# Kernel tuning notes

Measured on AMD Instinct MI355X. Metric: run time of the kernel, lower is better.

Reference implementation:

```python
import jax, jax.numpy as jnp
import numpy as np

B, N, C, H = 8, 1024, 256, 8   # graphs, nodes per graph, channels, heads
E = 131072                      # edges (avg degree 16)
DK = C // H
EPS = 1e-5


def setup_inputs() -> dict:
    key = jax.random.key(0)
    ks = jax.random.split(key, 16)
    s = 1.0 / np.sqrt(C)
    d = {
        'x': jax.random.normal(ks[0], (B * N, C), jnp.float32),
        'edge_index': jax.random.randint(ks[1], (2, E), 0, B * N, dtype=jnp.int64),
        'sph': jax.random.uniform(ks[2], (B, 1, N, N), jnp.float32),
        # local conv (GraphConv-style): root + neighbor linear
        'Wr': jax.random.normal(ks[3], (C, C), jnp.float32) * s,
        'Wn': jax.random.normal(ks[4], (C, C), jnp.float32) * s,
        # attention in/out projections (4 Linears as in MultiheadAttention)
        'Wq': jax.random.normal(ks[5], (C, C), jnp.float32) * s,
        'bq': jnp.zeros((C,), jnp.float32),
        'Wk': jax.random.normal(ks[6], (C, C), jnp.float32) * s,
        'bk': jnp.zeros((C,), jnp.float32),
        'Wv': jax.random.normal(ks[7], (C, C), jnp.float32) * s,
        'bv': jnp.zeros((C,), jnp.float32),
        'Wo': jax.random.normal(ks[8], (C, C), jnp.float32) * s,
        'bo': jnp.zeros((C,), jnp.float32),
        # MLP: C -> 2C -> C
        'W1': jax.random.normal(ks[9], (C, 2 * C), jnp.float32) * s,
        'b1': jnp.zeros((2 * C,), jnp.float32),
        'W2': jax.random.normal(ks[10], (2 * C, C), jnp.float32) * (1.0 / np.sqrt(2 * C)),
        'b2': jnp.zeros((C,), jnp.float32),
        # three batch norms (affine)
        'gamma1': jnp.ones((C,), jnp.float32), 'beta1': jnp.zeros((C,), jnp.float32),
        'gamma2': jnp.ones((C,), jnp.float32), 'beta2': jnp.zeros((C,), jnp.float32),
        'gamma3': jnp.ones((C,), jnp.float32), 'beta3': jnp.zeros((C,), jnp.float32),
    }
    return d


def _bn(h, g, b):
    # BatchNorm1d (training mode): per-feature stats over all nodes
    m = h.mean(axis=0)
    v = h.var(axis=0)
    return (h - m) * jax.lax.rsqrt(v + EPS) * g + b


def reference(x, edge_index, sph, Wr, Wn, Wq, bq, Wk, bk, Wv, bv, Wo, bo,
              W1, b1, W2, b2, gamma1, beta1, gamma2, beta2, gamma3, beta3):
    src, dst = edge_index[0], edge_index[1]

    # 1) local MPNN branch: h = conv(x) + x, then norm1
    msg = (x @ Wn)[src]                                   # [E, C]
    agg = jax.ops.segment_sum(msg, dst, num_segments=B * N)
    h1 = _bn(x @ Wr + agg + x, gamma1, beta1)             # [BN, C]

    # 2) global sph-modulated attention branch (dense batch is a reshape:
    #    equal-size graphs -> mask all True)
    hd = x.reshape(B, N, C)
    q = (hd @ Wq + bq).reshape(B, N, H, DK).transpose(0, 2, 1, 3)  # [B,H,N,DK]
    k = (hd @ Wk + bk).reshape(B, N, H, DK).transpose(0, 2, 1, 3)
    v = (hd @ Wv + bv).reshape(B, N, H, DK).transpose(0, 2, 1, 3)
    scores = jnp.einsum('bhnd,bhmd->bhnm', q, k) * (1.0 / np.sqrt(DK))
    scores = scores * sph                                  # structural modulation
    p = jax.nn.softmax(scores, axis=-1)
    o = jnp.einsum('bhnm,bhmd->bhnd', p, v)                # [B,H,N,DK]
    o = o.transpose(0, 2, 1, 3).reshape(B * N, C) @ Wo + bo
    h2 = _bn(o + x, gamma2, beta2)

    # 3) sum branches, MLP residual, norm3
    out = h1 + h2
    out = out + (jax.nn.relu(out @ W1 + b1) @ W2 + b2)
    return _bn(out, gamma3, beta3)
```

## Files before the change

### kernel.cpp

```cpp
#include <hip/hip_runtime.h>
#include <hip/hip_bf16.h>

constexpr int Bg  = 8;
constexpr int Nn  = 1024;
constexpr int Cc  = 256;
constexpr int Hh  = 8;
constexpr int DKh = 32;
constexpr int Ee  = 131072;
constexpr int BNn = Bg * Nn;
#define EPSV 1e-5f

typedef __attribute__((ext_vector_type(8))) short bf16x8;
typedef __attribute__((ext_vector_type(4))) float f32x4;

static __device__ __forceinline__ unsigned short f2b(float v) {
    __hip_bfloat16 h = __float2bfloat16(v);
    return __builtin_bit_cast(unsigned short, h);
}
static __device__ __forceinline__ float b2f(unsigned short u) {
    unsigned int x = ((unsigned int)u) << 16;
    return __builtin_bit_cast(float, x);
}
static __device__ __forceinline__ bf16x8 ldb8(const unsigned short* p) {
    return *(const bf16x8*)p;
}

__global__ __launch_bounds__(256) void prep_k(
    const float* __restrict__ x, unsigned short* __restrict__ xcat,
    const float* __restrict__ Wr, const float* __restrict__ Wn,
    const float* __restrict__ Wq, const float* __restrict__ Wk,
    const float* __restrict__ Wv, const float* __restrict__ Wo,
    const float* __restrict__ W1, const float* __restrict__ W2,
    unsigned short* __restrict__ WcatT,
    unsigned short* __restrict__ WqT, unsigned short* __restrict__ WkT,
    unsigned short* __restrict__ WvT, unsigned short* __restrict__ WoT,
    unsigned short* __restrict__ W1T, unsigned short* __restrict__ W2T,
    const int* __restrict__ ei, int* __restrict__ deg)
{
    int blk = blockIdx.x;
    if (blk < 2048) {
        int i = (blk * 256 + threadIdx.x) * 4;
        float4 v = *(const float4*)(x + i);
        int r = i >> 8, c = i & 255;
        ushort4 pk;
        pk.x = f2b(v.x); pk.y = f2b(v.y); pk.z = f2b(v.z); pk.w = f2b(v.w);
        *(ushort4*)(xcat + (size_t)r * 512 + c) = pk;
    } else if (blk < 4608) {
        int idx = (blk - 2048) * 256 + threadIdx.x;
        if (idx < 131072) {
            int n = idx >> 9, k = idx & 511;
            float v = (k < 256) ? Wr[k * 256 + n] : Wn[(k - 256) * 256 + n];
            WcatT[((size_t)(n >> 4) * 16 + (k >> 5)) * 512 + (n & 15) * 32 + (k & 31)] = f2b(v);
        } else if (idx < 393216) {
            int l = idx - 131072;
            int wsel = l >> 16; l &= 65535;
            int n = l >> 8, kk = l & 255;
            const float* S = wsel == 0 ? Wq : wsel == 1 ? Wk : wsel == 2 ? Wv : Wo;
            unsigned short* D = wsel == 0 ? WqT : wsel == 1 ? WkT : wsel == 2 ? WvT : WoT;
            D[((size_t)(n >> 4) * 8 + (kk >> 5)) * 512 + (n & 15) * 32 + (kk & 31)]
                = f2b(S[kk * 256 + n]);
        } else if (idx < 524288) {
            int l = idx - 393216;
            int n = l >> 8, kk = l & 255;
            W1T[((size_t)(n >> 4) * 8 + (kk >> 5)) * 512 + (n & 15) * 32 + (kk & 31)]
                = f2b(W1[kk * 512 + n]);
        } else {
            int l = idx - 524288;
            int n = l >> 9, kk = l & 511;
            W2T[((size_t)(n >> 4) * 16 + (kk >> 5)) * 512 + (n & 15) * 32 + (kk & 31)]
                = f2b(W2[kk * 256 + n]);
        }
    } else {
        int e = (blk - 4608) * 256 + threadIdx.x;
        atomicAdd(&deg[ei[Ee + e]], 1);
    }
}

__global__ __launch_bounds__(256) void scan_k(
    const int* __restrict__ deg, int* __restrict__ rowst, int* __restrict__ cursor)
{
    __shared__ int partial[256];
    int t = threadIdx.x;
    int local[32];
    int s = 0;
    #pragma unroll
    for (int i = 0; i < 32; ++i) { local[i] = deg[i * 256 + t]; s += local[i]; }
    partial[t] = s;
    __syncthreads();
    for (int off = 1; off < 256; off <<= 1) {
        int v = (t >= off) ? partial[t - off] : 0;
        __syncthreads();
        partial[t] += v;
        __syncthreads();
    }
    int base = partial[t] - s;
    #pragma unroll
    for (int i = 0; i < 32; ++i) {
        int n = i * 256 + t;
        rowst[n] = base;
        cursor[n] = base;
        base += local[i];
    }
}

__global__ __launch_bounds__(256) void place_k(
    const int* __restrict__ ei, int* __restrict__ cursor, int* __restrict__ eidx)
{
    int e = blockIdx.x * 256 + threadIdx.x;
    int s = ei[e], d = ei[Ee + e];
    int pos = atomicAdd(&cursor[d], 1);
    eidx[pos] = s;
}

__global__ __launch_bounds__(256, 4) void gather_qkv_k(
    const float* __restrict__ x, const int* __restrict__ rowst,
    const int* __restrict__ deg, const int* __restrict__ eidx,
    unsigned short* __restrict__ xcat,
    const unsigned short* __restrict__ WT,
    const float* __restrict__ bq, const float* __restrict__ bk,
    const float* __restrict__ bv,
    unsigned short* __restrict__ qb, unsigned short* __restrict__ kb,
    unsigned short* __restrict__ vTb, float qscale)
{
    __shared__ unsigned short vtile[64][40];
    int blk = blockIdx.x;

    if (blk < 2048) {
        int n = blk * 4 + (threadIdx.x >> 6);
        int c4 = (threadIdx.x & 63) * 4;
        int b0 = rowst[n], d = deg[n];
        float4 acc = {0.f, 0.f, 0.f, 0.f};
        int i = 0;
        for (; i + 4 <= d; i += 4) {
            int s0 = eidx[b0 + i], s1 = eidx[b0 + i + 1];
            int s2 = eidx[b0 + i + 2], s3 = eidx[b0 + i + 3];
            ushort4 a0 = *(const ushort4*)(xcat + (size_t)s0 * 512 + c4);
            ushort4 a1 = *(const ushort4*)(xcat + (size_t)s1 * 512 + c4);
            ushort4 a2 = *(const ushort4*)(xcat + (size_t)s2 * 512 + c4);
            ushort4 a3 = *(const ushort4*)(xcat + (size_t)s3 * 512 + c4);
            acc.x += (b2f(a0.x) + b2f(a1.x)) + (b2f(a2.x) + b2f(a3.x));
            acc.y += (b2f(a0.y) + b2f(a1.y)) + (b2f(a2.y) + b2f(a3.y));
            acc.z += (b2f(a0.z) + b2f(a1.z)) + (b2f(a2.z) + b2f(a3.z));
            acc.w += (b2f(a0.w) + b2f(a1.w)) + (b2f(a2.w) + b2f(a3.w));
        }
        for (; i < d; ++i) {
            int s = eidx[b0 + i];
            ushort4 a = *(const ushort4*)(xcat + (size_t)s * 512 + c4);
            acc.x += b2f(a.x); acc.y += b2f(a.y);
            acc.z += b2f(a.z); acc.w += b2f(a.w);
        }
        ushort4 pk;
        pk.x = f2b(acc.x); pk.y = f2b(acc.y); pk.z = f2b(acc.z); pk.w = f2b(acc.w);
        *(ushort4*)(xcat + (size_t)n * 512 + 256 + c4) = pk;
        return;
    }

    int qblk = blk - 2048;
    const int n0 = (qblk % 12) * 64;
    const int m0 = (qblk / 12) * 32;
    const int t = threadIdx.x;
    const int wave = t >> 6, lane = t & 63;
    const int tl = lane & 15, g = lane >> 4;
    const int wr = wave >> 1, wc = wave & 1;
    const int which = n0 >> 8;
    const int lda = 512;

    f32x4 acc[2] = {};

    const unsigned short* a0 = xcat + (size_t)(m0 + wr * 16 + tl) * lda + g * 8;
    const unsigned short* b0 = WT + ((size_t)(n0 >> 4) + wc * 2) * 8 * 512 + tl * 32 + g * 8;
    const unsigned short* b1 = b0 + 8 * 512;

    for (int k0 = 0; k0 < 256; k0 += 32) {
        bf16x8 af  = ldb8(a0 + k0);
        bf16x8 bf0 = ldb8(b0 + (k0 >> 5) * 512), bf1 = ldb8(b1 + (k0 >> 5) * 512);
        acc[0] = __builtin_amdgcn_mfma_f32_16x16x32_bf16(af, bf0, acc[0], 0, 0, 0);
        acc[1] = __builtin_amdgcn_mfma_f32_16x16x32_bf16(af, bf1, acc[1], 0, 0, 0);
    }

    const float* bias = which == 0 ? bq : which == 1 ? bk : bv;
    const float sc = which == 0 ? qscale : 1.f;

    if (which == 0) {
        #pragma unroll
        for (int c16 = 0; c16 < 2; ++c16)
            #pragma unroll
            for (int reg = 0; reg < 4; ++reg) {
                int row = m0 + wr * 16 + g * 4 + reg;
                int col = (n0 & 255) + wc * 32 + c16 * 16 + tl;
                qb[(size_t)row * Cc + col] = f2b((acc[c16][reg] + bias[col]) * sc);
            }
    } else if (which == 1) {
        #pragma unroll
        for (int c16 = 0; c16 < 2; ++c16)
            #pragma unroll
            for (int reg = 0; reg < 4; ++reg) {
                int row = m0 + wr * 16 + g * 4 + reg;
                int col = (n0 & 255) + wc * 32 + c16 * 16 + tl;
                kb[((size_t)(row >> 4) * 8 + (col >> 5)) * 512
                   + (row & 15) * 32 + (col & 31)] = f2b(acc[c16][reg] + bias[col]);
            }
    } else {
        #pragma unroll
        for (int c16 = 0; c16 < 2; ++c16)
            #pragma unroll
            for (int reg = 0; reg < 4; ++reg) {
                int colL = wc * 32 + c16 * 16 + tl;
                int rowL = wr * 16 + g * 4 + reg;
                vtile[colL][rowL] = f2b(acc[c16][reg] + bias[(n0 & 255) + colL]);
            }
        __syncthreads();
        int clocal = t >> 2, q4 = t & 3;
        int colg = (n0 & 255) + clocal;
        int hh = colg >> 5, dd = colg & 31;
        int bg = m0 >> 10;
        int m_loc = (m0 & 1023) + q4 * 8;
        int mt64 = m_loc >> 6, ks = (m_loc >> 5) & 1, gg = (m_loc >> 3) & 3;
        int cg = dd >> 4, tlv = dd & 15;
        ushort4 u0 = *(ushort4*)&vtile[clocal][q4 * 8];
        ushort4 u1 = *(ushort4*)&vtile[clocal][q4 * 8 + 4];
        unsigned short* dst = vTb
            + (((size_t)(bg * Hh + hh) * 16 + mt64) * 2048)
            + ((size_t)((ks * 2 + cg) * 16 + tlv) * 32) + gg * 8;
        *(ushort4*)dst = u0;
        *(ushort4*)(dst + 4) = u1;
    }
}

__global__ __launch_bounds__(512, 8) void attn_h1_k(
    const unsigned short* __restrict__ q, const unsigned short* __restrict__ k,
    const unsigned short* __restrict__ vT, const float* __restrict__ sph,
    unsigned short* __restrict__ op0,
    const unsigned short* __restrict__ xcat, const unsigned short* __restrict__ WcatT,
    const float* __restrict__ x, unsigned short* __restrict__ h1preb,
    float* __restrict__ gsum, float* __restrict__ gsq)
{
    __shared__ float Sph[2][16][132];
    __shared__ unsigned short Ps[Hh][16][72];
    float* csum = (float*)&Ps[0][0][0];
    float* csq  = csum + 256;

    const int blk = blockIdx.x;
    const int t = threadIdx.x;
    const int wave = t >> 6;
    const int lane = t & 63;
    const int tl = lane & 15, g = lane >> 4;

    if (blk < 512) {
        const int b  = blk & 7;
        const int n0 = (blk >> 3) * 16;
        const int w  = wave;

        bf16x8 qf = ldb8(q + ((size_t)(b * Nn + n0 + tl)) * Cc + w * DKh + g * 8);

        float lsum = 0.f;
        f32x4 oacc[2] = {};

        const unsigned short* kfb = k + ((size_t)(b * 512 + w)) * 512 + tl * 32 + g * 8;
        const unsigned short* vfb = vT + ((size_t)(b * Hh + w) * 16) * 2048
                                     + (size_t)tl * 32 + g * 8;
        const float* sbase = sph + ((size_t)b * Nn + n0) * Nn;

        if (t < 256) {
            int r1 = t >> 4, c1 = (t & 15) * 8;
            const float* src = sbase + (size_t)r1 * Nn + c1;
            *(float4*)&Sph[0][r1][c1]     = *(const float4*)src;
            *(float4*)&Sph[0][r1][c1 + 4] = *(const float4*)(src + 4);
        }
        __syncthreads();

        int cur = 0;
        for (int it = 0; it < 8; ++it) {
            const int m0 = it * 128;
            if (it < 7 && t < 256) {
                int r1 = t >> 4, c1 = (t & 15) * 8;
                const float* src = sbase + (size_t)r1 * Nn + m0 + 128 + c1;
                *(float4*)&Sph[cur ^ 1][r1][c1]     = *(const float4*)src;
                *(float4*)&Sph[cur ^ 1][r1][c1 + 4] = *(const float4*)(src + 4);
            }

            #pragma unroll
            for (int half = 0; half < 2; ++half) {
                const int mh = m0 + half * 64;

                f32x4 st[4];
                #pragma unroll
                for (int mg = 0; mg < 4; ++mg) {
                    bf16x8 ka = ldb8(kfb + (size_t)((mh >> 4) + mg) * 4096);
                    f32x4 z = {0.f, 0.f, 0.f, 0.f};
                    st[mg] = __builtin_amdgcn_mfma_f32_16x16x32_bf16(ka, qf, z, 0, 0, 0);
                }

                #pragma unroll
                for (int mg = 0; mg < 4; ++mg) {
                    float4 sp = *(const float4*)&Sph[cur][tl][half * 64 + mg * 16 + g * 4];
                    float p0 = __builtin_amdgcn_exp2f(st[mg][0] * sp.x);
                    float p1 = __builtin_amdgcn_exp2f(st[mg][1] * sp.y);
                    float p2 = __builtin_amdgcn_exp2f(st[mg][2] * sp.z);
                    float p3 = __builtin_amdgcn_exp2f(st[mg][3] * sp.w);
                    lsum += (p0 + p1) + (p2 + p3);
                    ushort4 pk;
                    pk.x = f2b(p0); pk.y = f2b(p1); pk.z = f2b(p2); pk.w = f2b(p3);
                    *(ushort4*)&Ps[w][tl][mg * 16 + g * 4] = pk;
                }

                const unsigned short* vtile64 = vfb + (size_t)(mh >> 6) * 2048;
                #pragma unroll
                for (int ks = 0; ks < 2; ++ks) {
                    bf16x8 pa = ldb8(&Ps[w][tl][ks * 32 + g * 8]);
                    #pragma unroll
                    for (int cg = 0; cg < 2; ++cg) {
                        bf16x8 vb = ldb8(vtile64 + (size_t)(ks * 2 + cg) * 512);
                        oacc[cg] = __builtin_amdgcn_mfma_f32_16x16x32_bf16(pa, vb, oacc[cg], 0, 0, 0);
                    }
                }
            }

            __syncthreads();
            cur ^= 1;
        }

        lsum += __shfl_xor(lsum, 16);
        lsum += __shfl_xor(lsum, 32);
        float* shl = (float*)&Ps[w][0][0];
        if (g == 0) shl[tl] = lsum;
        #pragma unroll
        for (int r = 0; r < 4; ++r) {
            float inv = 1.f / shl[g * 4 + r];
            #pragma unroll
            for (int cg = 0; cg < 2; ++cg)
                op0[((size_t)(b * Nn + n0 + g * 4 + r)) * Cc + w * DKh + cg * 16 + tl]
                    = f2b(oacc[cg][r] * inv);
        }
        return;
    }

    const int wrg = wave >> 2;
    const int wcg = wave & 3;
    const int m0g = (blk - 512) * 32;
    const int N = Cc;

    if (t < 256) { csum[t] = 0.f; csq[t] = 0.f; }
    __syncthreads();

    f32x4 acc[4] = {};

    const unsigned short* a0 = xcat + (size_t)(m0g + wrg * 16 + tl) * 512 + g * 8;
    const unsigned short* bb = WcatT + (size_t)(wcg * 4) * 16 * 512 + tl * 32 + g * 8;

    for (int k0 = 0; k0 < 512; k0 += 32) {
        bf16x8 af = ldb8(a0 + k0);
        #pragma unroll
        for (int c16 = 0; c16 < 4; ++c16) {
            bf16x8 bf = ldb8(bb + ((size_t)c16 * 16 + (k0 >> 5)) * 512);
            acc[c16] = __builtin_amdgcn_mfma_f32_16x16x32_bf16(af, bf, acc[c16], 0, 0, 0);
        }
    }

    #pragma unroll
    for (int c16 = 0; c16 < 4; ++c16) {
        int col = wcg * 64 + c16 * 16 + tl;
        float ls = 0.f, lq = 0.f;
        #pragma unroll
        for (int reg = 0; reg < 4; ++reg) {
            int row = m0g + wrg * 16 + g * 4 + reg;
            size_t idx = (size_t)row * N + col;
            float v = acc[c16][reg] + x[idx];
            ls += v; lq += v * v;
            h1preb[idx] = f2b(v);
        }
        atomicAdd(&csum[col], ls);
        atomicAdd(&csq[col],  lq);
    }
    __syncthreads();
    if (t < 256) {
        atomicAdd(&gsum[t], csum[t]);
        atomicAdd(&gsq[t],  csq[t]);
    }
}

template<int TAG>
__global__ __launch_bounds__(256, 4) void gemm_mfma_k(
    const unsigned short* __restrict__ A, const unsigned short* __restrict__ WT,
    const float* __restrict__ bias, const unsigned short* __restrict__ addb,
    float* __restrict__ outf, unsigned short* __restrict__ outb,
    float* __restrict__ gsum, float* __restrict__ gsq,
    int M, int K, int lda, int N, int relu, float oscale)
{
    const int t = threadIdx.x;
    const int wave = t >> 6, lane = t & 63;
    const int tl = lane & 15, g = lane >> 4;
    const int wr = wave >> 1, wc = wave & 1;
    const int m0 = blockIdx.y * 32, n0 = blockIdx.x * 64;

    __shared__ float csum[64], csq[64];
    if (gsum) {
        if (t < 64) { csum[t] = 0.f; csq[t] = 0.f; }
        __syncthreads();
    }

    f32x4 acc[2] = {};

    const int kt = K >> 5;
    const unsigned short* a0 = A  + (size_t)(m0 + wr * 16 + tl) * lda + g * 8;
    const unsigned short* b0 = WT + ((size_t)(n0 >> 4) + wc * 2) * kt * 512 + tl * 32 + g * 8;
    const unsigned short* b1 = b0 + (size_t)kt * 512;

    for (int k0 = 0; k0 < K; k0 += 32) {
        bf16x8 af  = ldb8(a0 + k0);
        bf16x8 bf0 = ldb8(b0 + (k0 >> 5) * 512), bf1 = ldb8(b1 + (k0 >> 5) * 512);
        acc[0] = __builtin_amdgcn_mfma_f32_16x16x32_bf16(af, bf0, acc[0], 0, 0, 0);
        acc[1] = __builtin_amdgcn_mfma_f32_16x16x32_bf16(af, bf1, acc[1], 0, 0, 0);
    }

    #pragma unroll
    for (int c16 = 0; c16 < 2; ++c16) {
        int colL = wc * 32 + c16 * 16 + tl;
        int col  = n0 + colL;
        float ls = 0.f, lq = 0.f;
        #pragma unroll
        for (int reg = 0; reg < 4; ++reg) {
            int row = m0 + wr * 16 + g * 4 + reg;
            float v = acc[c16][reg];
            if (bias) v += bias[col];
            v *= oscale;
            size_t idx = (size_t)row * N + col;
            if (addb) v += b2f(addb[idx]);
            ls += v; lq += v * v;
            if (relu) v = fmaxf(v, 0.f);
            if (outf) outf[idx] = v;
            if (outb) outb[idx] = f2b(v);
        }
        if (gsum) { atomicAdd(&csum[colL], ls); atomicAdd(&csq[colL], lq); }
    }
    if (gsum) {
        __syncthreads();
        if (t < 64) {
            atomicAdd(&gsum[n0 + t], csum[t]);
            atomicAdd(&gsq[n0 + t],  csq[t]);
        }
    }
}

__global__ __launch_bounds__(256, 4) void gemm_attnA_k(
    const unsigned short* __restrict__ op0,
    const unsigned short* __restrict__ WT, const float* __restrict__ bias,
    const float* __restrict__ add1, unsigned short* __restrict__ h2preb,
    float* __restrict__ gsum, float* __restrict__ gsq)
{
    const int K = Cc, N = Cc;
    const int t = threadIdx.x;
    const int wave = t >> 6, lane = t & 63;
    const int tl = lane & 15, g = lane >> 4;
    const int wr = wave >> 1, wc = wave & 1;
    const int m0 = blockIdx.y * 32, n0 = blockIdx.x * 64;

    __shared__ float csum[64], csq[64];
    if (t < 64) { csum[t] = 0.f; csq[t] = 0.f; }
    __syncthreads();

    f32x4 acc[2] = {};

    const int arow = m0 + wr * 16 + tl;
    const unsigned short* a0b = op0 + (size_t)arow * K + g * 8;
    const unsigned short* b0 = WT + ((size_t)(n0 >> 4) + wc * 2) * 8 * 512 + tl * 32 + g * 8;
    const unsigned short* b1 = b0 + 8 * 512;

    for (int k0 = 0; k0 < K; k0 += 32) {
        bf16x8 af  = ldb8(a0b + k0);
        bf16x8 bf0 = ldb8(b0 + (k0 >> 5) * 512), bf1 = ldb8(b1 + (k0 >> 5) * 512);
        acc[0] = __builtin_amdgcn_mfma_f32_16x16x32_bf16(af, bf0, acc[0], 0, 0, 0);
        acc[1] = __builtin_amdgcn_mfma_f32_16x16x32_bf16(af, bf1, acc[1], 0, 0, 0);
    }

    #pragma unroll
    for (int c16 = 0; c16 < 2; ++c16) {
        int colL = wc * 32 + c16 * 16 + tl;
        int col  = n0 + colL;
        float ls = 0.f, lq = 0.f;
        #pragma unroll
        for (int reg = 0; reg < 4; ++reg) {
            int row = m0 + wr * 16 + g * 4 + reg;
            float v = acc[c16][reg] + bias[col];
            size_t idx = (size_t)row * N + col;
            v += add1[idx];
            ls += v; lq += v * v;
            h2preb[idx] = f2b(v);
        }
        atomicAdd(&csum[colL], ls); atomicAdd(&csq[colL], lq);
    }
    __syncthreads();
    if (t < 64) {
        atomicAdd(&gsum[n0 + t], csum[t]);
        atomicAdd(&gsq[n0 + t],  csq[t]);
    }
}

__global__ __launch_bounds__(256) void bn_apply_k(
    const float* __restrict__ h, const float* __restrict__ gsum,
    const float* __restrict__ gsq, const float* __restrict__ gamma,
    const float* __restrict__ beta, float* __restrict__ outf)
{
    size_t i4 = ((size_t)blockIdx.x * 256 + threadIdx.x) * 4;
    int ch = (int)(i4 & (Cc - 1));
    float4 hv = *(const float4*)(h + i4);
    float4 sm = *(const float4*)(gsum + ch);
    float4 sq = *(const float4*)(gsq + ch);
    float4 ga = *(const float4*)(gamma + ch);
    float4 be = *(const float4*)(beta + ch);
    float4 o;
    {
        float m = sm.x * (1.f / BNn), var = sq.x * (1.f / BNn) - m * m;
        o.x = (hv.x - m) * rsqrtf(var + EPSV) * ga.x + be.x;
    }
    {
        float m = sm.y * (1.f / BNn), var = sq.y * (1.f / BNn) - m * m;
        o.y = (hv.y - m) * rsqrtf(var + EPSV) * ga.y + be.y;
    }
    {
        float m = sm.z * (1.f / BNn), var = sq.z * (1.f / BNn) - m * m;
        o.z = (hv.z - m) * rsqrtf(var + EPSV) * ga.z + be.z;
    }
    {
        float m = sm.w * (1.f / BNn), var = sq.w * (1.f / BNn) - m * m;
        o.w = (hv.w - m) * rsqrtf(var + EPSV) * ga.w + be.w;
    }
    *(float4*)(outf + i4) = o;
}

__global__ __launch_bounds__(256) void bn_apply12_k(
    const unsigned short* __restrict__ h1preb, const unsigned short* __restrict__ h2preb,
    const float* __restrict__ stats,
    const float* __restrict__ g1, const float* __restrict__ be1,
    const float* __restrict__ g2, const float* __restrict__ be2,
    unsigned short* __restrict__ outb)
{
    size_t i4 = ((size_t)blockIdx.x * 256 + threadIdx.x) * 4;
    int ch = (int)(i4 & (Cc - 1));
    ushort4 u1 = *(const ushort4*)(h1preb + i4);
    ushort4 u2 = *(const ushort4*)(h2preb + i4);
    float4 s1m = *(const float4*)(stats + ch);
    float4 s1q = *(const float4*)(stats + 256 + ch);
    float4 s2m = *(const float4*)(stats + 512 + ch);
    float4 s2q = *(const float4*)(stats + 768 + ch);
    float4 G1 = *(const float4*)(g1 + ch),  B1 = *(const float4*)(be1 + ch);
    float4 G2 = *(const float4*)(g2 + ch),  B2 = *(const float4*)(be2 + ch);
    ushort4 pk;
    #define BN12C(comp, ucomp) { \
        float m1 = s1m.comp * (1.f / BNn), v1 = s1q.comp * (1.f / BNn) - m1 * m1; \
        float m2 = s2m.comp * (1.f / BNn), v2 = s2q.comp * (1.f / BNn) - m2 * m2; \
        float o = (b2f(u1.ucomp) - m1) * rsqrtf(v1 + EPSV) * G1.comp + B1.comp \
                + (b2f(u2.ucomp) - m2) * rsqrtf(v2 + EPSV) * G2.comp + B2.comp; \
        pk.ucomp = f2b(o); }
    BN12C(x, x) BN12C(y, y) BN12C(z, z) BN12C(w, w)
    #undef BN12C
    *(ushort4*)(outb + i4) = pk;
}

extern "C" void kernel_launch(void* const* d_in, const int* in_sizes, int n_in,
                              void* d_out, int out_size, void* d_ws, size_t ws_size,
                              hipStream_t stream)
{
    const float* x   = (const float*)d_in[0];
    const int*   ei  = (const int*)  d_in[1];
    const float* sph = (const float*)d_in[2];
    const float* Wr  = (const float*)d_in[3];
    const float* Wn  = (const float*)d_in[4];
    const float* Wq  = (const float*)d_in[5];
    const float* bq  = (const float*)d_in[6];
    const float* Wk  = (const float*)d_in[7];
    const float* bk  = (const float*)d_in[8];
    const float* Wv  = (const float*)d_in[9];
    const float* bv  = (const float*)d_in[10];
    const float* Wo  = (const float*)d_in[11];
    const float* bo  = (const float*)d_in[12];
    const float* W1  = (const float*)d_in[13];
    const float* b1  = (const float*)d_in[14];
    const float* W2  = (const float*)d_in[15];
    const float* b2  = (const float*)d_in[16];
    const float* g1  = (const float*)d_in[17];
    const float* be1 = (const float*)d_in[18];
    const float* g2  = (const float*)d_in[19];
    const float* be2 = (const float*)d_in[20];
    const float* g3  = (const float*)d_in[21];
    const float* be3 = (const float*)d_in[22];
    float* out = (float*)d_out;

    const size_t SL = (size_t)BNn * Cc;

    float* ws = (float*)d_ws;
    float* s1 = ws;
    float* s2 = s1 + SL;
    float* s3 = s2 + SL;

    int*   deg      = (int*)(s3 + SL);
    float* statsAll = (float*)(deg + 8192);
    int*   rowst    = (int*)(statsAll + 1536);
    int*   cursor   = rowst + 8256;
    int*   eidx     = cursor + 8192;

    unsigned short* xcat = (unsigned short*)(eidx + 131072);
    unsigned short* qb   = xcat + 2 * SL;
    unsigned short* kb   = qb + SL;
    unsigned short* vTb  = kb + SL;
    unsigned short* osb  = kb;
    unsigned short* hid  = xcat;

    unsigned short* WcatT = vTb + SL;
    unsigned short* WqT   = WcatT + 131072;
    unsigned short* WkT   = WqT + 65536;
    unsigned short* WvT   = WkT + 65536;
    unsigned short* WoT   = WvT + 65536;
    unsigned short* W1T   = WoT + 65536;
    unsigned short* W2T   = W1T + 131072;
    unsigned short* op0b   = (unsigned short*)s1;
    unsigned short* h1preb = (unsigned short*)s2;
    unsigned short* h2preb = (unsigned short*)s3;

    dim3 gN256(4, 256);
    dim3 gN512(8, 256);

    const float QSCALE = 0.17677669529663687f * 1.4426950408889634f;

    hipMemsetAsync(deg, 0, (8192 + 1536) * sizeof(float), stream);
    prep_k<<<5120, 256, 0, stream>>>(x, xcat, Wr, Wn, Wq, Wk, Wv, Wo, W1, W2,
                                     WcatT, WqT, WkT, WvT, WoT, W1T, W2T, ei, deg);
    scan_k<<<1, 256, 0, stream>>>(deg, rowst, cursor);
    place_k<<<Ee / 256, 256, 0, stream>>>(ei, cursor, eidx);
    gather_qkv_k<<<5120, 256, 0, stream>>>(x, rowst, deg, eidx, xcat,
                                           WqT, bq, bk, bv, qb, kb, vTb, QSCALE);
    attn_h1_k<<<768, 512, 0, stream>>>(qb, kb, vTb, sph, op0b,
                                       xcat, WcatT, x, h1preb,
                                       statsAll, statsAll + 256);
    gemm_attnA_k<<<gN256, 256, 0, stream>>>(op0b, WoT, bo, x,
                                            h2preb, statsAll + 512, statsAll + 768);
    bn_apply12_k<<<(int)(SL / 1024), 256, 0, stream>>>(h1preb, h2preb, statsAll,
                                                       g1, be1, g2, be2, osb);
    gemm_mfma_k<1><<<gN512, 256, 0, stream>>>(osb, W1T, b1, nullptr,
                                              nullptr, hid, nullptr, nullptr,
                                              BNn, Cc, Cc, 2 * Cc, 1, 1.f);
    gemm_mfma_k<2><<<gN256, 256, 0, stream>>>(hid, W2T, b2, osb,
                                              s2, nullptr, statsAll + 1024, statsAll + 1280,
                                              BNn, 2 * Cc, 2 * Cc, Cc, 0, 1.f);
    bn_apply_k<<<(int)(SL / 1024), 256, 0, stream>>>(s2, statsAll + 1024,
                                                     statsAll + 1280, g3, be3, out);
}
```

Measured before the change: 302.1 us.

## Store bf16 activations in MFMA-fragment tiled layout across all GEMM operands

Activations that feed MFMA GEMMs (x concat with aggregated neighbours, attention output, normalised sum, MLP hidden) are now written in a 16-row by 32-column tiled layout, so each lane's 8-element A-fragment load comes from one contiguous 512-element tile. A separate row-major bf16 copy of x is kept for the neighbour gather, and the generic GEMM template is split into two specialised MLP kernels with the runtime branches removed. The intent is more coalesced A-operand loads and less epilogue overhead, at the cost of scattered, narrower writes in the producer epilogues and an extra x copy.

Result: faster. 282.9 us (median of 3 runs) (-6.4%).

```diff
diff --git a/kernel.cpp b/kernel.cpp
--- a/kernel.cpp
+++ b/kernel.cpp
@@ -10,6 +10,7 @@
 constexpr int BNn = Bg * Nn;
 #define EPSV 1e-5f
 
+
 typedef __attribute__((ext_vector_type(8))) short bf16x8;
 typedef __attribute__((ext_vector_type(4))) float f32x4;
 
@@ -26,7 +27,8 @@
 }
 
 __global__ __launch_bounds__(256) void prep_k(
-    const float* __restrict__ x, unsigned short* __restrict__ xcat,
+    const float* __restrict__ x, unsigned short* __restrict__ xf,
+    unsigned short* __restrict__ xlo,
     const float* __restrict__ Wr, const float* __restrict__ Wn,
     const float* __restrict__ Wq, const float* __restrict__ Wk,
     const float* __restrict__ Wv, const float* __restrict__ Wo,
@@ -44,7 +46,9 @@
         int r = i >> 8, c = i & 255;
         ushort4 pk;
         pk.x = f2b(v.x); pk.y = f2b(v.y); pk.z = f2b(v.z); pk.w = f2b(v.w);
-        *(ushort4*)(xcat + (size_t)r * 512 + c) = pk;
+        *(ushort4*)(xlo + (size_t)r * 256 + c) = pk;
+        *(ushort4*)(xf + ((size_t)(r >> 4) * 16 + (c >> 5)) * 512
+                    + (r & 15) * 32 + (c & 31)) = pk;
     } else if (blk < 4608) {
         int idx = (blk - 2048) * 256 + threadIdx.x;
         if (idx < 131072) {
@@ -113,9 +117,9 @@
 }
 
 __global__ __launch_bounds__(256, 4) void gather_qkv_k(
-    const float* __restrict__ x, const int* __restrict__ rowst,
+    const unsigned short* __restrict__ xlo, const int* __restrict__ rowst,
     const int* __restrict__ deg, const int* __restrict__ eidx,
-    unsigned short* __restrict__ xcat,
+    unsigned short* __restrict__ xf,
     const unsigned short* __restrict__ WT,
     const float* __restrict__ bq, const float* __restrict__ bk,
     const float* __restrict__ bv,
@@ -134,10 +138,10 @@
         for (; i + 4 <= d; i += 4) {
             int s0 = eidx[b0 + i], s1 = eidx[b0 + i + 1];
             int s2 = eidx[b0 + i + 2], s3 = eidx[b0 + i + 3];
-            ushort4 a0 = *(const ushort4*)(xcat + (size_t)s0 * 512 + c4);
-            ushort4 a1 = *(const ushort4*)(xcat + (size_t)s1 * 512 + c4);
-            ushort4 a2 = *(const ushort4*)(xcat + (size_t)s2 * 512 + c4);
-            ushort4 a3 = *(const ushort4*)(xcat + (size_t)s3 * 512 + c4);
+            ushort4 a0 = *(const ushort4*)(xlo + (size_t)s0 * 256 + c4);
+            ushort4 a1 = *(const ushort4*)(xlo + (size_t)s1 * 256 + c4);
+            ushort4 a2 = *(const ushort4*)(xlo + (size_t)s2 * 256 + c4);
+            ushort4 a3 = *(const ushort4*)(xlo + (size_t)s3 * 256 + c4);
             acc.x += (b2f(a0.x) + b2f(a1.x)) + (b2f(a2.x) + b2f(a3.x));
             acc.y += (b2f(a0.y) + b2f(a1.y)) + (b2f(a2.y) + b2f(a3.y));
             acc.z += (b2f(a0.z) + b2f(a1.z)) + (b2f(a2.z) + b2f(a3.z));
@@ -145,13 +149,15 @@
         }
         for (; i < d; ++i) {
             int s = eidx[b0 + i];
-            ushort4 a = *(const ushort4*)(xcat + (size_t)s * 512 + c4);
+            ushort4 a = *(const ushort4*)(xlo + (size_t)s * 256 + c4);
             acc.x += b2f(a.x); acc.y += b2f(a.y);
             acc.z += b2f(a.z); acc.w += b2f(a.w);
         }
         ushort4 pk;
         pk.x = f2b(acc.x); pk.y = f2b(acc.y); pk.z = f2b(acc.z); pk.w = f2b(acc.w);
-        *(ushort4*)(xcat + (size_t)n * 512 + 256 + c4) = pk;
+        int cg2 = 256 + c4;
+        *(ushort4*)(xf + ((size_t)(n >> 4) * 16 + (cg2 >> 5)) * 512
+                    + (n & 15) * 32 + (cg2 & 31)) = pk;
         return;
     }
 
@@ -163,16 +169,15 @@
     const int tl = lane & 15, g = lane >> 4;
     const int wr = wave >> 1, wc = wave & 1;
     const int which = n0 >> 8;
-    const int lda = 512;
 
     f32x4 acc[2] = {};
 
-    const unsigned short* a0 = xcat + (size_t)(m0 + wr * 16 + tl) * lda + g * 8;
+    const unsigned short* a0 = xf + (size_t)((m0 >> 4) + wr) * 16 * 512 + tl * 32 + g * 8;
     const unsigned short* b0 = WT + ((size_t)(n0 >> 4) + wc * 2) * 8 * 512 + tl * 32 + g * 8;
     const unsigned short* b1 = b0 + 8 * 512;
 
     for (int k0 = 0; k0 < 256; k0 += 32) {
-        bf16x8 af  = ldb8(a0 + k0);
+        bf16x8 af  = ldb8(a0 + (k0 >> 5) * 512);
         bf16x8 bf0 = ldb8(b0 + (k0 >> 5) * 512), bf1 = ldb8(b1 + (k0 >> 5) * 512);
         acc[0] = __builtin_amdgcn_mfma_f32_16x16x32_bf16(af, bf0, acc[0], 0, 0, 0);
         acc[1] = __builtin_amdgcn_mfma_f32_16x16x32_bf16(af, bf1, acc[1], 0, 0, 0);
@@ -231,7 +236,7 @@
     const unsigned short* __restrict__ q, const unsigned short* __restrict__ k,
     const unsigned short* __restrict__ vT, const float* __restrict__ sph,
     unsigned short* __restrict__ op0,
-    const unsigned short* __restrict__ xcat, const unsigned short* __restrict__ WcatT,
+    const unsigned short* __restrict__ xf, const unsigned short* __restrict__ WcatT,
     const float* __restrict__ x, unsigned short* __restrict__ h1preb,
     float* __restrict__ gsum, float* __restrict__ gsq)
 {
@@ -324,12 +329,13 @@
         lsum += __shfl_xor(lsum, 32);
         float* shl = (float*)&Ps[w][0][0];
         if (g == 0) shl[tl] = lsum;
+        const size_t rt = (size_t)((b * Nn + n0) >> 4);
         #pragma unroll
         for (int r = 0; r < 4; ++r) {
             float inv = 1.f / shl[g * 4 + r];
             #pragma unroll
             for (int cg = 0; cg < 2; ++cg)
-                op0[((size_t)(b * Nn + n0 + g * 4 + r)) * Cc + w * DKh + cg * 16 + tl]
+                op0[(rt * 8 + w) * 512 + (g * 4 + r) * 32 + cg * 16 + tl]
                     = f2b(oacc[cg][r] * inv);
         }
         return;
@@ -345,11 +351,11 @@
 
     f32x4 acc[4] = {};
 
-    const unsigned short* a0 = xcat + (size_t)(m0g + wrg * 16 + tl) * 512 + g * 8;
+    const unsigned short* a0 = xf + (size_t)((m0g >> 4) + wrg) * 16 * 512 + tl * 32 + g * 8;
     const unsigned short* bb = WcatT + (size_t)(wcg * 4) * 16 * 512 + tl * 32 + g * 8;
 
     for (int k0 = 0; k0 < 512; k0 += 32) {
-        bf16x8 af = ldb8(a0 + k0);
+        bf16x8 af = ldb8(a0 + (k0 >> 5) * 512);
         #pragma unroll
         for (int c16 = 0; c16 < 4; ++c16) {
             bf16x8 bf = ldb8(bb + ((size_t)c16 * 16 + (k0 >> 5)) * 512);
@@ -379,13 +385,11 @@
     }
 }
 
-template<int TAG>
-__global__ __launch_bounds__(256, 4) void gemm_mfma_k(
-    const unsigned short* __restrict__ A, const unsigned short* __restrict__ WT,
-    const float* __restrict__ bias, const unsigned short* __restrict__ addb,
-    float* __restrict__ outf, unsigned short* __restrict__ outb,
-    float* __restrict__ gsum, float* __restrict__ gsq,
-    int M, int K, int lda, int N, int relu, float oscale)
+__global__ __launch_bounds__(256, 4) void mlp1_k(
+    const unsigned short* __restrict__ A,
+    const unsigned short* __restrict__ WT,
+    const float* __restrict__ bias,
+    unsigned short* __restrict__ outb)
 {
     const int t = threadIdx.x;
     const int wave = t >> 6, lane = t & 63;
@@ -393,52 +397,85 @@
     const int wr = wave >> 1, wc = wave & 1;
     const int m0 = blockIdx.y * 32, n0 = blockIdx.x * 64;
 
-    __shared__ float csum[64], csq[64];
-    if (gsum) {
-        if (t < 64) { csum[t] = 0.f; csq[t] = 0.f; }
-        __syncthreads();
-    }
-
     f32x4 acc[2] = {};
 
-    const int kt = K >> 5;
-    const unsigned short* a0 = A  + (size_t)(m0 + wr * 16 + tl) * lda + g * 8;
-    const unsigned short* b0 = WT + ((size_t)(n0 >> 4) + wc * 2) * kt * 512 + tl * 32 + g * 8;
-    const unsigned short* b1 = b0 + (size_t)kt * 512;
-
-    for (int k0 = 0; k0 < K; k0 += 32) {
-        bf16x8 af  = ldb8(a0 + k0);
+    const unsigned short* a0 = A  + (size_t)((m0 >> 4) + wr) * 8 * 512 + tl * 32 + g * 8;
+    const unsigned short* b0 = WT + ((size_t)(n0 >> 4) + wc * 2) * 8 * 512 + tl * 32 + g * 8;
+    const unsigned short* b1 = b0 + 8 * 512;
+
+    for (int k0 = 0; k0 < 256; k0 += 32) {
+        bf16x8 af  = ldb8(a0 + (k0 >> 5) * 512);
         bf16x8 bf0 = ldb8(b0 + (k0 >> 5) * 512), bf1 = ldb8(b1 + (k0 >> 5) * 512);
         acc[0] = __builtin_amdgcn_mfma_f32_16x16x32_bf16(af, bf0, acc[0], 0, 0, 0);
         acc[1] = __builtin_amdgcn_mfma_f32_16x16x32_bf16(af, bf1, acc[1], 0, 0, 0);
     }
 
+    const size_t rtO = (size_t)(m0 >> 4) + wr;
+    #pragma unroll
+    for (int c16 = 0; c16 < 2; ++c16) {
+        int col  = n0 + wc * 32 + c16 * 16 + tl;
+        int ktO  = col >> 5;
+        #pragma unroll
+        for (int reg = 0; reg < 4; ++reg) {
+            float v = fmaxf(acc[c16][reg] + bias[col], 0.f);
+            outb[(rtO * 16 + ktO) * 512 + (g * 4 + reg) * 32 + (col & 31)] = f2b(v);
+        }
+    }
+}
+
+__global__ __launch_bounds__(256, 4) void mlp2_k(
+    const unsigned short* __restrict__ A,
+    const unsigned short* __restrict__ WT,
+    const float* __restrict__ bias,
+    const unsigned short* __restrict__ addb,
+    float* __restrict__ outf,
+    float* __restrict__ gsum, float* __restrict__ gsq)
+{
+    const int N = Cc;
+    const int t = threadIdx.x;
+    const int wave = t >> 6, lane = t & 63;
+    const int tl = lane & 15, g = lane >> 4;
+    const int wr = wave >> 1, wc = wave & 1;
+    const int m0 = blockIdx.y * 32, n0 = blockIdx.x * 64;
+
+    __shared__ float csum[64], csq[64];
+    if (t < 64) { csum[t] = 0.f; csq[t] = 0.f; }
+    __syncthreads();
+
+    f32x4 acc[2] = {};
+
+    const unsigned short* a0 = A  + (size_t)((m0 >> 4) + wr) * 16 * 512 + tl * 32 + g * 8;
+    const unsigned short* b0 = WT + ((size_t)(n0 >> 4) + wc * 2) * 16 * 512 + tl * 32 + g * 8;
+    const unsigned short* b1 = b0 + 16 * 512;
+
+    for (int k0 = 0; k0 < 512; k0 += 32) {
+        bf16x8 af  = ldb8(a0 + (k0 >> 5) * 512);
+        bf16x8 bf0 = ldb8(b0 + (k0 >> 5) * 512), bf1 = ldb8(b1 + (k0 >> 5) * 512);
+        acc[0] = __builtin_amdgcn_mfma_f32_16x16x32_bf16(af, bf0, acc[0], 0, 0, 0);
+        acc[1] = __builtin_amdgcn_mfma_f32_16x16x32_bf16(af, bf1, acc[1], 0, 0, 0);
+    }
+
+    const size_t rtR = (size_t)(m0 >> 4) + wr;
     #pragma unroll
     for (int c16 = 0; c16 < 2; ++c16) {
         int colL = wc * 32 + c16 * 16 + tl;
         int col  = n0 + colL;
+        int ktR  = col >> 5;
         float ls = 0.f, lq = 0.f;
         #pragma unroll
         for (int reg = 0; reg < 4; ++reg) {
             int row = m0 + wr * 16 + g * 4 + reg;
-            float v = acc[c16][reg];
-            if (bias) v += bias[col];
-            v *= oscale;
-            size_t idx = (size_t)row * N + col;
-            if (addb) v += b2f(addb[idx]);
+            float v = acc[c16][reg] + bias[col]
+                    + b2f(addb[(rtR * 8 + ktR) * 512 + (g * 4 + reg) * 32 + (col & 31)]);
             ls += v; lq += v * v;
-            if (relu) v = fmaxf(v, 0.f);
-            if (outf) outf[idx] = v;
-            if (outb) outb[idx] = f2b(v);
-        }
-        if (gsum) { atomicAdd(&csum[colL], ls); atomicAdd(&csq[colL], lq); }
-    }
-    if (gsum) {
-        __syncthreads();
-        if (t < 64) {
-            atomicAdd(&gsum[n0 + t], csum[t]);
-            atomicAdd(&gsq[n0 + t],  csq[t]);
-        }
+            outf[(size_t)row * N + col] = v;
+        }
+        atomicAdd(&csum[colL], ls); atomicAdd(&csq[colL], lq);
+    }
+    __syncthreads();
+    if (t < 64) {
+        atomicAdd(&gsum[n0 + t], csum[t]);
+        atomicAdd(&gsq[n0 + t],  csq[t]);
     }
 }
 
@@ -448,7 +485,7 @@
     const float* __restrict__ add1, unsigned short* __restrict__ h2preb,
     float* __restrict__ gsum, float* __restrict__ gsq)
 {
-    const int K = Cc, N = Cc;
+    const int N = Cc;
     const int t = threadIdx.x;
     const int wave = t >> 6, lane = t & 63;
     const int tl = lane & 15, g = lane >> 4;
@@ -461,13 +498,12 @@
 
     f32x4 acc[2] = {};
 
-    const int arow = m0 + wr * 16 + tl;
-    const unsigned short* a0b = op0 + (size_t)arow * K + g * 8;
+    const unsigned short* a0b = op0 + (size_t)((m0 >> 4) + wr) * 8 * 512 + tl * 32 + g * 8;
     const unsigned short* b0 = WT + ((size_t)(n0 >> 4) + wc * 2) * 8 * 512 + tl * 32 + g * 8;
     const unsigned short* b1 = b0 + 8 * 512;
 
-    for (int k0 = 0; k0 < K; k0 += 32) {
-        bf16x8 af  = ldb8(a0b + k0);
+    for (int k0 = 0; k0 < 256; k0 += 32) {
+        bf16x8 af  = ldb8(a0b + (k0 >> 5) * 512);
         bf16x8 bf0 = ldb8(b0 + (k0 >> 5) * 512), bf1 = ldb8(b1 + (k0 >> 5) * 512);
         acc[0] = __builtin_amdgcn_mfma_f32_16x16x32_bf16(af, bf0, acc[0], 0, 0, 0);
         acc[1] = __builtin_amdgcn_mfma_f32_16x16x32_bf16(af, bf1, acc[1], 0, 0, 0);
@@ -554,7 +590,9 @@
         pk.ucomp = f2b(o); }
     BN12C(x, x) BN12C(y, y) BN12C(z, z) BN12C(w, w)
     #undef BN12C
-    *(ushort4*)(outb + i4) = pk;
+    int row = (int)(i4 >> 8), col = ch;
+    *(ushort4*)(outb + ((size_t)(row >> 4) * 8 + (col >> 5)) * 512
+                + (row & 15) * 32 + (col & 31)) = pk;
 }
 
 extern "C" void kernel_launch(void* const* d_in, const int* in_sizes, int n_in,
@@ -599,12 +637,12 @@
     int*   cursor   = rowst + 8256;
     int*   eidx     = cursor + 8192;
 
-    unsigned short* xcat = (unsigned short*)(eidx + 131072);
-    unsigned short* qb   = xcat + 2 * SL;
-    unsigned short* kb   = qb + SL;
-    unsigned short* vTb  = kb + SL;
-    unsigned short* osb  = kb;
-    unsigned short* hid  = xcat;
+    unsigned short* xf  = (unsigned short*)(eidx + 131072);
+    unsigned short* qb  = xf + 2 * SL;
+    unsigned short* kb  = qb + SL;
+    unsigned short* vTb = kb + SL;
+    unsigned short* osb = kb;
+    unsigned short* hid = xf;
 
     unsigned short* WcatT = vTb + SL;
     unsigned short* WqT   = WcatT + 131072;
@@ -613,6 +651,7 @@
     unsigned short* WoT   = WvT + 65536;
     unsigned short* W1T   = WoT + 65536;
     unsigned short* W2T   = W1T + 131072;
+    unsigned short* xlo   = W2T + 131072;
     unsigned short* op0b   = (unsigned short*)s1;
     unsigned short* h1preb = (unsigned short*)s2;
     unsigned short* h2preb = (unsigned short*)s3;
@@ -623,25 +662,22 @@
     const float QSCALE = 0.17677669529663687f * 1.4426950408889634f;
 
     hipMemsetAsync(deg, 0, (8192 + 1536) * sizeof(float), stream);
-    prep_k<<<5120, 256, 0, stream>>>(x, xcat, Wr, Wn, Wq, Wk, Wv, Wo, W1, W2,
+    prep_k<<<5120, 256, 0, stream>>>(x, xf, xlo, Wr, Wn, Wq, Wk, Wv, Wo, W1, W2,
                                      WcatT, WqT, WkT, WvT, WoT, W1T, W2T, ei, deg);
     scan_k<<<1, 256, 0, stream>>>(deg, rowst, cursor);
     place_k<<<Ee / 256, 256, 0, stream>>>(ei, cursor, eidx);
-    gather_qkv_k<<<5120, 256, 0, stream>>>(x, rowst, deg, eidx, xcat,
+    gather_qkv_k<<<5120, 256, 0, stream>>>(xlo, rowst, deg, eidx, xf,
                                            WqT, bq, bk, bv, qb, kb, vTb, QSCALE);
     attn_h1_k<<<768, 512, 0, stream>>>(qb, kb, vTb, sph, op0b,
-                                       xcat, WcatT, x, h1preb,
+                                       xf, WcatT, x, h1preb,
                                        statsAll, statsAll + 256);
     gemm_attnA_k<<<gN256, 256, 0, stream>>>(op0b, WoT, bo, x,
                                             h2preb, statsAll + 512, statsAll + 768);
     bn_apply12_k<<<(int)(SL / 1024), 256, 0, stream>>>(h1preb, h2preb, statsAll,
                                                        g1, be1, g2, be2, osb);
-    gemm_mfma_k<1><<<gN512, 256, 0, stream>>>(osb, W1T, b1, nullptr,
-                                              nullptr, hid, nullptr, nullptr,
-                                              BNn, Cc, Cc, 2 * Cc, 1, 1.f);
-    gemm_mfma_k<2><<<gN256, 256, 0, stream>>>(hid, W2T, b2, osb,
-                                              s2, nullptr, statsAll + 1024, statsAll + 1280,
-                                              BNn, 2 * Cc, 2 * Cc, Cc, 0, 1.f);
+    mlp1_k<<<gN512, 256, 0, stream>>>(osb, W1T, b1, hid);
+    mlp2_k<<<gN256, 256, 0, stream>>>(hid, W2T, b2, osb, s2,
+                                      statsAll + 1024, statsAll + 1280);
     bn_apply_k<<<(int)(SL / 1024), 256, 0, stream>>>(s2, statsAll + 1024,
                                                      statsAll + 1280, g3, be3, out);
 }
```
